# Performance work log

Measured on AMD Instinct MI355X. Metric: run time of the kernel, lower is better.

## Reference

```python
import jax, jax.numpy as jnp
import numpy as np

NA = 100000   # author nodes
NP = 100000   # paper nodes
E = 500000    # edges per relation
H = 128       # hidden size
FA = 256      # author input features
FP = 128      # paper input features
LA = 4        # author labels
LP = 7        # paper labels


def setup_inputs() -> dict:
    key = jax.random.key(0)
    ks = iter(jax.random.split(key, 48))
    def rn(shape, scale=0.05):
        return jax.random.normal(next(ks), shape, jnp.float32) * scale
    inp = {}
    inp['x_author'] = jax.random.normal(next(ks), (NA, FA), jnp.float32)
    inp['x_paper'] = jax.random.normal(next(ks), (NP, FP), jnp.float32)
    inp['edge_index_p2a'] = jax.random.randint(next(ks), (2, E), 0, 100000, jnp.int64)  # row0: paper src, row1: author dst
    inp['edge_index_a2p'] = jax.random.randint(next(ks), (2, E), 0, 100000, jnp.int64)  # row0: author src, row1: paper dst
    # layer 1 convs (per message type): lin_src, lin_dst, lin_update(2H->H)
    inp['w1_p2a_src'] = rn((FP, H)); inp['b1_p2a_src'] = rn((H,))
    inp['w1_p2a_dst'] = rn((FA, H)); inp['b1_p2a_dst'] = rn((H,))
    inp['w1_p2a_upd'] = rn((2 * H, H)); inp['b1_p2a_upd'] = rn((H,))
    inp['w1_a2p_src'] = rn((FA, H)); inp['b1_a2p_src'] = rn((H,))
    inp['w1_a2p_dst'] = rn((FP, H)); inp['b1_a2p_dst'] = rn((H,))
    inp['w1_a2p_upd'] = rn((2 * H, H)); inp['b1_a2p_upd'] = rn((H,))
    # layer 2 convs (all dims = H)
    inp['w2_p2a_src'] = rn((H, H)); inp['b2_p2a_src'] = rn((H,))
    inp['w2_p2a_dst'] = rn((H, H)); inp['b2_p2a_dst'] = rn((H,))
    inp['w2_p2a_upd'] = rn((2 * H, H)); inp['b2_p2a_upd'] = rn((H,))
    inp['w2_a2p_src'] = rn((H, H)); inp['b2_a2p_src'] = rn((H,))
    inp['w2_a2p_dst'] = rn((H, H)); inp['b2_a2p_dst'] = rn((H,))
    inp['w2_a2p_upd'] = rn((2 * H, H)); inp['b2_a2p_upd'] = rn((H,))
    # batchnorm affine params per node type per layer
    inp['g1_a'] = jnp.ones((H,), jnp.float32); inp['be1_a'] = jnp.zeros((H,), jnp.float32)
    inp['g1_p'] = jnp.ones((H,), jnp.float32); inp['be1_p'] = jnp.zeros((H,), jnp.float32)
    inp['g2_a'] = jnp.ones((H,), jnp.float32); inp['be2_a'] = jnp.zeros((H,), jnp.float32)
    inp['g2_p'] = jnp.ones((H,), jnp.float32); inp['be2_p'] = jnp.zeros((H,), jnp.float32)
    # post message-passing heads
    inp['w_post_a'] = rn((H, LA)); inp['b_post_a'] = rn((LA,))
    inp['w_post_p'] = rn((H, LP)); inp['b_post_p'] = rn((LP,))
    return inp


def _mean_agg(x_src, src, dst, n_dst):
    # gather source features along edges, mean-scatter to destination nodes
    msg = x_src[src]                                            # [E, F]
    s = jax.ops.segment_sum(msg, dst, num_segments=n_dst)       # [n_dst, F]
    cnt = jax.ops.segment_sum(jnp.ones((dst.shape[0],), msg.dtype), dst, num_segments=n_dst)
    return s / jnp.maximum(cnt, 1.0)[:, None]


def _conv(x_src, x_dst, src, dst, ws, bs, wd, bd, wu, bu):
    agg = _mean_agg(x_src, src, dst, x_dst.shape[0])
    h = jnp.concatenate([x_dst @ wd + bd, agg @ ws + bs], axis=-1)   # [n_dst, 2H]
    return h @ wu + bu


def _bn_lrelu(x, g, b):
    # BatchNorm1d(eps=1) in training mode (batch stats, biased var) then LeakyReLU(0.01)
    m = x.mean(axis=0)
    v = x.var(axis=0)
    y = g * (x - m) / jnp.sqrt(v + 1.0) + b
    return jnp.where(y >= 0, y, 0.01 * y)


def reference(x_author, x_paper, edge_index_p2a, edge_index_a2p,
              w1_p2a_src, b1_p2a_src, w1_p2a_dst, b1_p2a_dst, w1_p2a_upd, b1_p2a_upd,
              w1_a2p_src, b1_a2p_src, w1_a2p_dst, b1_a2p_dst, w1_a2p_upd, b1_a2p_upd,
              w2_p2a_src, b2_p2a_src, w2_p2a_dst, b2_p2a_dst, w2_p2a_upd, b2_p2a_upd,
              w2_a2p_src, b2_a2p_src, w2_a2p_dst, b2_a2p_dst, w2_a2p_upd, b2_a2p_upd,
              g1_a, be1_a, g1_p, be1_p, g2_a, be2_a, g2_p, be2_p,
              w_post_a, b_post_a, w_post_p, b_post_p):
    src_pa, dst_pa = edge_index_p2a[0], edge_index_p2a[1]
    src_ap, dst_ap = edge_index_a2p[0], edge_index_a2p[1]
    # layer 1: per-message-type conv -> per-node-type BN + LeakyReLU
    h_a = _conv(x_paper, x_author, src_pa, dst_pa, w1_p2a_src, b1_p2a_src, w1_p2a_dst, b1_p2a_dst, w1_p2a_upd, b1_p2a_upd)
    h_p = _conv(x_author, x_paper, src_ap, dst_ap, w1_a2p_src, b1_a2p_src, w1_a2p_dst, b1_a2p_dst, w1_a2p_upd, b1_a2p_upd)
    h_a = _bn_lrelu(h_a, g1_a, be1_a)
    h_p = _bn_lrelu(h_p, g1_p, be1_p)
    # layer 2
    h_a2 = _conv(h_p, h_a, src_pa, dst_pa, w2_p2a_src, b2_p2a_src, w2_p2a_dst, b2_p2a_dst, w2_p2a_upd, b2_p2a_upd)
    h_p2 = _conv(h_a, h_p, src_ap, dst_ap, w2_a2p_src, b2_a2p_src, w2_a2p_dst, b2_a2p_dst, w2_a2p_upd, b2_a2p_upd)
    h_a2 = _bn_lrelu(h_a2, g2_a, be2_a)
    h_p2 = _bn_lrelu(h_p2, g2_p, be2_p)
    # post message-passing heads per node type
    out_a = h_a2 @ w_post_a + b_post_a   # [NA, LA]
    out_p = h_p2 @ w_post_p + b_post_p   # [NP, LP]
    return (out_a, out_p)
```

## Files before the change

kernel.cpp:

```cpp
#include <hip/hip_runtime.h>

#define NN 100000
#define NE 500000
#define HD 128
#define NBLK 391

typedef float f32x4v __attribute__((ext_vector_type(4)));
typedef short s16x8  __attribute__((ext_vector_type(8)));

static __device__ __forceinline__ unsigned f2bf_bits(float f){
  unsigned u = __float_as_uint(f);
  return (u + 0x7FFF + ((u >> 16) & 1)) >> 16;
}

static __device__ __forceinline__ void split8(const float* a, s16x8& hi, s16x8& lo){
  #pragma unroll
  for (int j = 0; j < 8; ++j){
    float f = a[j];
    unsigned hb = f2bf_bits(f);
    float hf = __uint_as_float(hb << 16);
    float lf = f - hf;
    hi[j] = (short)hb;
    lo[j] = (short)f2bf_bits(lf);
  }
}

static __device__ __forceinline__ float4 bn_lrelu4(float4 v, float4 sc, float4 sh){
  v.x = v.x*sc.x + sh.x; v.x = v.x >= 0.f ? v.x : 0.01f*v.x;
  v.y = v.y*sc.y + sh.y; v.y = v.y >= 0.f ? v.y : 0.01f*v.y;
  v.z = v.z*sc.z + sh.z; v.z = v.z >= 0.f ? v.z : 0.01f*v.z;
  v.w = v.w*sc.w + sh.w; v.w = v.w >= 0.f ? v.w : 0.01f*v.w;
  return v;
}

__global__ void k_count(const int* __restrict__ ei_pa, const int* __restrict__ ei_ap,
                        int* __restrict__ deg2){
  int idx = blockIdx.x * 256 + threadIdx.x;
  if (idx < NE)        atomicAdd(&deg2[      ei_pa[NE + idx]], 1);
  else if (idx < 2*NE) atomicAdd(&deg2[NN + ei_ap[NE + (idx - NE)]], 1);
}

__global__ void k_bsum(const int* __restrict__ deg2, int* __restrict__ bsum){
  int rel = blockIdx.x / NBLK, b = blockIdx.x % NBLK;
  int i = b*256 + threadIdx.x;
  int v = (i < NN) ? deg2[rel*NN + i] : 0;
  __shared__ int s[256];
  s[threadIdx.x] = v; __syncthreads();
  for (int o = 128; o > 0; o >>= 1){
    if (threadIdx.x < o) s[threadIdx.x] += s[threadIdx.x + o];
    __syncthreads();
  }
  if (threadIdx.x == 0) bsum[rel*512 + b] = s[0];
}

__global__ void k_bscan(const int* __restrict__ bsum, int* __restrict__ bsoff){
  int rel = blockIdx.x, t = threadIdx.x;
  int v = (t < NBLK) ? bsum[rel*512 + t] : 0;
  __shared__ int s[512];
  s[t] = v; __syncthreads();
  for (int o = 1; o < 512; o <<= 1){
    int x = (t >= o) ? s[t - o] : 0;
    __syncthreads();
    s[t] += x;
    __syncthreads();
  }
  bsoff[rel*512 + t] = s[t] - v;
}

__global__ void k_scanC(const int* __restrict__ deg2, const int* __restrict__ bsoff,
                        int* __restrict__ off2, int* __restrict__ cur2){
  int rel = blockIdx.x / NBLK, b = blockIdx.x % NBLK;
  int i = b*256 + threadIdx.x, t = threadIdx.x;
  int v = (i < NN) ? deg2[rel*NN + i] : 0;
  __shared__ int s[256];
  s[t] = v; __syncthreads();
  for (int o = 1; o < 256; o <<= 1){
    int x = (t >= o) ? s[t - o] : 0;
    __syncthreads();
    s[t] += x;
    __syncthreads();
  }
  if (i < NN){
    int o = bsoff[rel*512 + b] + s[t] - v;
    off2[rel*NN + i] = o;
    cur2[rel*NN + i] = o;
  }
}

__global__ void k_fill(const int* __restrict__ ei_pa, const int* __restrict__ ei_ap,
                       int* __restrict__ cur2,
                       int* __restrict__ col_pa, int* __restrict__ col_ap){
  int idx = blockIdx.x * 256 + threadIdx.x;
  if (idx < NE){
    int s = ei_pa[idx], d = ei_pa[NE + idx];
    int pos = atomicAdd(&cur2[d], 1);
    col_pa[pos] = s;
  } else if (idx < 2*NE){
    int e = idx - NE;
    int s = ei_ap[e], d = ei_ap[NE + e];
    int pos = atomicAdd(&cur2[NN + d], 1);
    col_ap[pos] = s;
  }
}

struct FoldDesc { const float* A; const float* B; short* T; int off; };
struct FoldArgs { FoldDesc d[8]; int rs[9]; };

__global__ void k_fold(FoldArgs fa){
  int row = blockIdx.x;
  int seg = 0;
  #pragma unroll
  for (int s = 0; s < 8; ++s) if (row >= fa.rs[s+1]) seg = s + 1;
  int m = row - fa.rs[seg];
  const float* A = fa.d[seg].A + (size_t)m * 128;
  const float* B = fa.d[seg].B;
  int n = threadIdx.x;
  float acc = 0.f;
  for (int k = 0; k < 128; ++k) acc += A[k] * B[k*128 + n];
  unsigned hb = f2bf_bits(acc);
  float hf = __uint_as_float(hb << 16);
  unsigned lb = f2bf_bits(acc - hf);
  int gkc = fa.d[seg].off + (m >> 5), quad = (m >> 3) & 3, j = m & 7;
  int lane = quad*16 + (n & 15), nt = n >> 4;
  size_t fb = (size_t)((gkc*8 + nt)*2)*512 + lane*8 + j;
  fa.d[seg].T[fb]       = (short)hb;
  fa.d[seg].T[fb + 512] = (short)lb;
}

struct BiasArgs { const float* bd[4]; const float* bs[4]; const float* wu[4];
                  const float* bu[4]; float* outb[4]; };
__global__ void k_biasfold(BiasArgs ba){
  int s = blockIdx.x, j = threadIdx.x;
  const float* wu = ba.wu[s];
  float acc = ba.bu[s][j];
  for (int k = 0; k < 128; ++k)
    acc += ba.bd[s][k] * wu[k*128 + j] + ba.bs[s][k] * wu[(128 + k)*128 + j];
  ba.outb[s][j] = acc;
}

__global__ __launch_bounds__(256)
void k_gemm2(const float* __restrict__ A1, int lda1, int KC1,
             const float* __restrict__ bn1,
             const float* __restrict__ A2, int lda2, int KC2,
             const short* __restrict__ Bf,
             const float* __restrict__ bias, const float* __restrict__ extra,
             float* __restrict__ C, float* __restrict__ stats, int M)
{
  __shared__ __align__(16) char smem[32768];
  short* Bs = (short*)smem;

  const int tid  = threadIdx.x;
  const int wave = tid >> 6, lane = tid & 63;
  const int li   = lane & 15, quad = lane >> 4;
  const int rowT = blockIdx.x * 128 + wave * 32;
  const int KCtot = KC1 + KC2;

  f32x4v acc[2][8];
  #pragma unroll
  for (int mt = 0; mt < 2; ++mt)
    #pragma unroll
    for (int nt = 0; nt < 8; ++nt)
      acc[mt][nt] = (f32x4v){0.f, 0.f, 0.f, 0.f};

  float4 c0[2], c1[2], n0[2], n1[2];
  auto loadA = [&](int gkc, float4* p0, float4* p1){
    const float* Ab; int ld, kk; bool bn;
    if (gkc < KC1){ Ab = A1; ld = lda1; kk = gkc; bn = (bn1 != nullptr); }
    else          { Ab = A2; ld = lda2; kk = gkc - KC1; bn = false; }
    float4 sc0, sc1, sh0, sh1;
    if (bn){
      const float* bsc = bn1 + kk*32 + quad*8;
      sc0 = *(const float4*)bsc;        sc1 = *(const float4*)(bsc + 4);
      sh0 = *(const float4*)(bsc+128);  sh1 = *(const float4*)(bsc + 132);
    }
    #pragma unroll
    for (int mt = 0; mt < 2; ++mt){
      int row = rowT + mt*16 + li;
      if (row < M){
        const float* ap = Ab + (size_t)row*ld + kk*32 + quad*8;
        float4 v0 = *(const float4*)ap;
        float4 v1 = *(const float4*)(ap + 4);
        if (bn){ v0 = bn_lrelu4(v0, sc0, sh0); v1 = bn_lrelu4(v1, sc1, sh1); }
        p0[mt] = v0; p1[mt] = v1;
      } else {
        p0[mt] = make_float4(0.f,0.f,0.f,0.f);
        p1[mt] = make_float4(0.f,0.f,0.f,0.f);
      }
    }
  };
  loadA(0, c0, c1);

  for (int g = 0; g < KCtot; g += 2){
    if (g > 0) __syncthreads();
    const short* src = Bf + (size_t)g*8192;
    #pragma unroll
    for (int c2 = 0; c2 < 8; ++c2){
      int id = c2*256 + tid;
      *(s16x8*)(Bs + id*8) = *(const s16x8*)(src + id*8);
    }
    __syncthreads();
    #pragma unroll
    for (int kc = 0; kc < 2; ++kc){
      int gkc = g + kc;
      if (gkc + 1 < KCtot) loadA(gkc + 1, n0, n1);
      s16x8 ah[2], al[2];
      #pragma unroll
      for (int mt = 0; mt < 2; ++mt){
        float av[8] = {c0[mt].x, c0[mt].y, c0[mt].z, c0[mt].w,
                       c1[mt].x, c1[mt].y, c1[mt].z, c1[mt].w};
        split8(av, ah[mt], al[mt]);
      }
      #pragma unroll
      for (int nt = 0; nt < 8; ++nt){
        const short* bp = Bs + ((kc*8 + nt) << 10) + lane*8;
        s16x8 bh = *(const s16x8*)bp;
        s16x8 bl = *(const s16x8*)(bp + 512);
        #pragma unroll
        for (int mt = 0; mt < 2; ++mt){
          acc[mt][nt] = __builtin_amdgcn_mfma_f32_16x16x32_bf16(ah[mt], bh, acc[mt][nt], 0, 0, 0);
          acc[mt][nt] = __builtin_amdgcn_mfma_f32_16x16x32_bf16(al[mt], bh, acc[mt][nt], 0, 0, 0);
          acc[mt][nt] = __builtin_amdgcn_mfma_f32_16x16x32_bf16(ah[mt], bl, acc[mt][nt], 0, 0, 0);
        }
      }
      #pragma unroll
      for (int mt = 0; mt < 2; ++mt){ c0[mt] = n0[mt]; c1[mt] = n1[mt]; }
    }
  }

  __syncthreads();
  float* Cw = (float*)smem + wave*2048;
  int col4 = lane & 31;
  float4 bias4 = make_float4(0.f,0.f,0.f,0.f);
  if (bias) bias4 = ((const float4*)bias)[col4];
  float4 s1 = make_float4(0.f,0.f,0.f,0.f), s2 = s1;
  #pragma unroll
  for (int mt = 0; mt < 2; ++mt){
    #pragma unroll
    for (int r = 0; r < 4; ++r){
      int lr = quad*4 + r;
      #pragma unroll
      for (int nt = 0; nt < 8; ++nt){
        int c = nt*16 + li;
        int chunk = ((c >> 2) + 2*quad) & 31;
        Cw[lr*128 + chunk*4 + (c & 3)] = acc[mt][nt][r];
      }
    }
    #pragma unroll
    for (int i = 0; i < 8; ++i){
      int lr = i*2 + (lane >> 5);
      int grow = rowT + mt*16 + lr;
      if (grow >= M) continue;
      int chunk = (col4 + 2*(lr >> 2)) & 31;
      float4 v = *(const float4*)(Cw + lr*128 + chunk*4);
      v.x += bias4.x; v.y += bias4.y; v.z += bias4.z; v.w += bias4.w;
      if (extra){
        float4 e = ((const float4*)(extra + (size_t)grow*128))[col4];
        v.x += e.x; v.y += e.y; v.z += e.z; v.w += e.w;
      }
      ((float4*)(C + (size_t)grow*128))[col4] = v;
      s1.x += v.x; s1.y += v.y; s1.z += v.z; s1.w += v.w;
      s2.x += v.x*v.x; s2.y += v.y*v.y; s2.z += v.z*v.z; s2.w += v.w*v.w;
    }
  }
  if (stats){
    __syncthreads();
    float* Ss = (float*)smem;
    ((float4*)Ss)[tid*2]     = s1;
    ((float4*)Ss)[tid*2 + 1] = s2;
    __syncthreads();
    int c = tid & 127, kind = tid >> 7;
    int cc4 = c >> 2, comp = c & 3;
    float s = 0.f;
    #pragma unroll
    for (int wv = 0; wv < 4; ++wv)
      #pragma unroll
      for (int hf = 0; hf < 2; ++hf)
        s += Ss[(wv*64 + hf*32 + cc4)*8 + kind*4 + comp];
    atomicAdd(&stats[kind*128 + c], s);
  }
}

__global__ __launch_bounds__(256)
void k_agg(const float* __restrict__ t, const int* __restrict__ off,
           const int* __restrict__ deg, const int* __restrict__ col,
           float* __restrict__ o, const float* __restrict__ bn){
  int slot = threadIdx.x >> 5, col4 = threadIdx.x & 31;
  int d = blockIdx.x*8 + slot;
  if (d >= NN) return;
  float4 sc4, sh4;
  bool hasbn = (bn != nullptr);
  if (hasbn){ sc4 = ((const float4*)bn)[col4]; sh4 = ((const float4*)(bn+128))[col4]; }
  int s0 = off[d], cnt = deg[d];
  float4 a0 = make_float4(0.f,0.f,0.f,0.f), a1 = a0;
  int i = 0;
  for (; i + 4 <= cnt; i += 4){
    int sa = col[s0+i], sb = col[s0+i+1], sct = col[s0+i+2], sd = col[s0+i+3];
    float4 v0 = ((const float4*)(t + (size_t)sa*128))[col4];
    float4 v1 = ((const float4*)(t + (size_t)sb*128))[col4];
    float4 v2 = ((const float4*)(t + (size_t)sct*128))[col4];
    float4 v3 = ((const float4*)(t + (size_t)sd*128))[col4];
    if (hasbn){
      v0 = bn_lrelu4(v0, sc4, sh4); v1 = bn_lrelu4(v1, sc4, sh4);
      v2 = bn_lrelu4(v2, sc4, sh4); v3 = bn_lrelu4(v3, sc4, sh4);
    }
    a0.x += v0.x + v2.x; a0.y += v0.y + v2.y; a0.z += v0.z + v2.z; a0.w += v0.w + v2.w;
    a1.x += v1.x + v3.x; a1.y += v1.y + v3.y; a1.z += v1.z + v3.z; a1.w += v1.w + v3.w;
  }
  for (; i < cnt; ++i){
    int sa = col[s0+i];
    float4 v0 = ((const float4*)(t + (size_t)sa*128))[col4];
    if (hasbn) v0 = bn_lrelu4(v0, sc4, sh4);
    a0.x += v0.x; a0.y += v0.y; a0.z += v0.z; a0.w += v0.w;
  }
  float inv = 1.0f / (float)(cnt > 0 ? cnt : 1);
  float4 r;
  r.x = (a0.x + a1.x)*inv; r.y = (a0.y + a1.y)*inv;
  r.z = (a0.z + a1.z)*inv; r.w = (a0.w + a1.w)*inv;
  ((float4*)(o + (size_t)d*128))[col4] = r;
}

__global__ void k_bnprep(const float* __restrict__ stats, const float* __restrict__ g,
                         const float* __restrict__ b, float* __restrict__ sc, int M){
  int c = threadIdx.x;
  float invN = 1.0f / (float)M;
  float m  = stats[c] * invN;
  float var = stats[128 + c] * invN - m*m;
  float scale = g[c] / sqrtf(var + 1.0f);
  sc[c] = scale;
  sc[128 + c] = b[c] - m*scale;
}

template<int LC>
__global__ void k_head(const float* __restrict__ h, const float* __restrict__ bn,
                       const float* __restrict__ w, const float* __restrict__ b,
                       float* __restrict__ o, int M){
  __shared__ float ws[128*LC];
  __shared__ float bs[LC];
  __shared__ float bsc[256];
  for (int i = threadIdx.x; i < 128*LC; i += 256) ws[i] = w[i];
  if (threadIdx.x < LC) bs[threadIdx.x] = b[threadIdx.x];
  if (threadIdx.x < 256) bsc[threadIdx.x] = bn[threadIdx.x];
  __syncthreads();
  int r = blockIdx.x*256 + threadIdx.x;
  if (r >= M) return;
  float acc[LC];
  #pragma unroll
  for (int c = 0; c < LC; ++c) acc[c] = bs[c];
  const float4* hr = (const float4*)(h + (size_t)r*128);
  for (int k4 = 0; k4 < 32; ++k4){
    float4 v = hr[k4];
    float4 sc = ((const float4*)bsc)[k4];
    float4 sh = ((const float4*)bsc)[32 + k4];
    v = bn_lrelu4(v, sc, sh);
    int k = k4*4;
    #pragma unroll
    for (int c = 0; c < LC; ++c)
      acc[c] += v.x*ws[k*LC+c] + v.y*ws[(k+1)*LC+c] + v.z*ws[(k+2)*LC+c] + v.w*ws[(k+3)*LC+c];
  }
  #pragma unroll
  for (int c = 0; c < LC; ++c) o[(size_t)r*LC + c] = acc[c];
}

extern "C" void kernel_launch(void* const* d_in, const int* in_sizes, int n_in,
                              void* d_out, int out_size, void* d_ws, size_t ws_size,
                              hipStream_t stream) {
  const float* x_author = (const float*)d_in[0];
  const float* x_paper  = (const float*)d_in[1];
  const int*   ei_pa    = (const int*)d_in[2];
  const int*   ei_ap    = (const int*)d_in[3];

  char* p = (char*)d_ws;
  auto alloc = [&](size_t bytes) -> void* {
    void* r = (void*)p; p += (bytes + 255) & ~(size_t)255; return r;
  };
  short* T_l1a  = (short*)alloc(12u*16384);
  short* T_l1ps = (short*)alloc( 8u*16384);
  short* T_l1pd = (short*)alloc( 4u*16384);
  short* T_l2a  = (short*)alloc( 8u*16384);
  short* T_l2p  = (short*)alloc( 8u*16384);
  float* w1a_b = (float*)alloc(128*4);      float* w1p_b = (float*)alloc(128*4);
  float* w2a_b = (float*)alloc(128*4);      float* w2p_b = (float*)alloc(128*4);
  float* stats4 = (float*)alloc(4*256*4);
  float* bnsc4  = (float*)alloc(4*256*4);
  int* deg2  = (int*)alloc(2*NN*4);
  int* off2  = (int*)alloc(2*NN*4);
  int* cur2  = (int*)alloc(2*NN*4);
  int* col_pa = (int*)alloc(NE*4);
  int* col_ap = (int*)alloc(NE*4);
  int* bsum  = (int*)alloc(1024*4);
  int* bsoff = (int*)alloc(1024*4);
  const size_t NB = (size_t)NN * 128;
  float* B1 = (float*)alloc(NB*4);
  float* B2 = (float*)alloc(NB*4);
  float* B3 = (float*)alloc(NB*4);
  float* B4 = (float*)alloc(NB*4);

  hipMemsetAsync(deg2, 0, 2*NN*4, stream);
  hipMemsetAsync(stats4, 0, 4*256*4, stream);
  k_count<<<(2*NE + 255)/256, 256, 0, stream>>>(ei_pa, ei_ap, deg2);
  k_bsum <<<2*NBLK, 256, 0, stream>>>(deg2, bsum);
  k_bscan<<<2, 512, 0, stream>>>(bsum, bsoff);
  k_scanC<<<2*NBLK, 256, 0, stream>>>(deg2, bsoff, off2, cur2);
  k_fill <<<(2*NE + 255)/256, 256, 0, stream>>>(ei_pa, ei_ap, cur2, col_pa, col_ap);

  FoldArgs fa;
  const float* wu1a = (const float*)d_in[8];
  const float* wu1p = (const float*)d_in[14];
  const float* wu2a = (const float*)d_in[20];
  const float* wu2p = (const float*)d_in[26];
  fa.d[0] = { (const float*)d_in[6],  wu1a,           T_l1a,  0 };
  fa.d[1] = { (const float*)d_in[4],  wu1a + 128*128, T_l1a,  8 };
  fa.d[2] = { (const float*)d_in[10], wu1p + 128*128, T_l1ps, 0 };
  fa.d[3] = { (const float*)d_in[12], wu1p,           T_l1pd, 0 };
  fa.d[4] = { (const float*)d_in[18], wu2a,           T_l2a,  0 };
  fa.d[5] = { (const float*)d_in[16], wu2a + 128*128, T_l2a,  4 };
  fa.d[6] = { (const float*)d_in[24], wu2p,           T_l2p,  0 };
  fa.d[7] = { (const float*)d_in[22], wu2p + 128*128, T_l2p,  4 };
  int rows[8] = {256,128,256,128,128,128,128,128};
  fa.rs[0] = 0;
  for (int i = 0; i < 8; ++i) fa.rs[i+1] = fa.rs[i] + rows[i];
  k_fold<<<fa.rs[8], 128, 0, stream>>>(fa);

  BiasArgs ba;
  ba.bd[0]=(const float*)d_in[7];  ba.bs[0]=(const float*)d_in[5];  ba.wu[0]=wu1a; ba.bu[0]=(const float*)d_in[9];  ba.outb[0]=w1a_b;
  ba.bd[1]=(const float*)d_in[13]; ba.bs[1]=(const float*)d_in[11]; ba.wu[1]=wu1p; ba.bu[1]=(const float*)d_in[15]; ba.outb[1]=w1p_b;
  ba.bd[2]=(const float*)d_in[19]; ba.bs[2]=(const float*)d_in[17]; ba.wu[2]=wu2a; ba.bu[2]=(const float*)d_in[21]; ba.outb[2]=w2a_b;
  ba.bd[3]=(const float*)d_in[25]; ba.bs[3]=(const float*)d_in[23]; ba.wu[3]=wu2p; ba.bu[3]=(const float*)d_in[27]; ba.outb[3]=w2p_b;
  k_biasfold<<<4, 128, 0, stream>>>(ba);

  const int GG = (NN + 127)/128;
  const int AGG_GRID = (NN + 7)/8;
  const int* off_pa = off2;        const int* deg_pa = deg2;
  const int* off_ap = off2 + NN;   const int* deg_ap = deg2 + NN;
  float* st_a1 = stats4;       float* st_p1 = stats4 + 256;
  float* st_a2 = stats4 + 512; float* st_p2 = stats4 + 768;
  float* sc_a1 = bnsc4;        float* sc_p1 = bnsc4 + 256;
  float* sc_a2 = bnsc4 + 512;  float* sc_p2 = bnsc4 + 768;

  k_agg<<<AGG_GRID, 256, 0, stream>>>(x_paper, off_pa, deg_pa, col_pa, B4, nullptr);
  k_gemm2<<<GG, 256, 0, stream>>>(x_author, 256, 8, nullptr, B4, 128, 4, T_l1a,
                                  w1a_b, nullptr, B1, st_a1, NN);
  k_bnprep<<<1, 128, 0, stream>>>(st_a1, (const float*)d_in[28], (const float*)d_in[29], sc_a1, NN);

  k_gemm2<<<GG, 256, 0, stream>>>(x_author, 256, 8, nullptr, nullptr, 0, 0, T_l1ps,
                                  nullptr, nullptr, B3, nullptr, NN);
  k_agg<<<AGG_GRID, 256, 0, stream>>>(B3, off_ap, deg_ap, col_ap, B4, nullptr);
  k_gemm2<<<GG, 256, 0, stream>>>(x_paper, 128, 4, nullptr, nullptr, 0, 0, T_l1pd,
                                  w1p_b, B4, B2, st_p1, NN);
  k_bnprep<<<1, 128, 0, stream>>>(st_p1, (const float*)d_in[30], (const float*)d_in[31], sc_p1, NN);

  k_agg<<<AGG_GRID, 256, 0, stream>>>(B2, off_pa, deg_pa, col_pa, B4, sc_p1);
  k_gemm2<<<GG, 256, 0, stream>>>(B1, 128, 4, sc_a1, B4, 128, 4, T_l2a,
                                  w2a_b, nullptr, B3, st_a2, NN);
  k_bnprep<<<1, 128, 0, stream>>>(st_a2, (const float*)d_in[32], (const float*)d_in[33], sc_a2, NN);
  k_head<4><<<(NN + 255)/256, 256, 0, stream>>>(B3, sc_a2, (const float*)d_in[36],
                                                (const float*)d_in[37], (float*)d_out, NN);

  k_agg<<<AGG_GRID, 256, 0, stream>>>(B1, off_ap, deg_ap, col_ap, B4, sc_a1);
  k_gemm2<<<GG, 256, 0, stream>>>(B2, 128, 4, sc_p1, B4, 128, 4, T_l2p,
                                  w2p_b, nullptr, B3, st_p2, NN);
  k_bnprep<<<1, 128, 0, stream>>>(st_p2, (const float*)d_in[34], (const float*)d_in[35], sc_p2, NN);
  k_head<7><<<(NN + 255)/256, 256, 0, stream>>>(B3, sc_p2, (const float*)d_in[38],
                                                (const float*)d_in[39], (float*)d_out + (size_t)NN*4, NN);
}
```

Before: 862.0 us.

## Store intermediates as pre-split bf16 hi/lo pairs and stage B via LDS DMA

Intermediate activation buffers now hold each row as bf16 hi and lo halves instead of fp32. The GEMM can then feed MFMA directly without re-splitting in the inner loop, and aggregation reconstructs fp32 from the halves. BatchNorm+LeakyReLU is moved into a separate in-place pass (k_bnapply) rather than being applied inside agg and GEMM loads. B tiles are loaded with global_load_lds and A prefetch is restructured into double-buffered two-chunk phases. Total bytes per buffer are unchanged. The change adds extra kernel passes, and the split/reconstruct steps carry a small precision risk.

```diff
diff --git a/kernel.cpp b/kernel.cpp
--- a/kernel.cpp
+++ b/kernel.cpp
@@ -12,16 +12,32 @@
   unsigned u = __float_as_uint(f);
   return (u + 0x7FFF + ((u >> 16) & 1)) >> 16;
 }
-
-static __device__ __forceinline__ void split8(const float* a, s16x8& hi, s16x8& lo){
-  #pragma unroll
-  for (int j = 0; j < 8; ++j){
-    float f = a[j];
+static __device__ __forceinline__ float bfu(unsigned short u){
+  return __uint_as_float(((unsigned)u) << 16);
+}
+static __device__ __forceinline__ float4 recon4(ushort4 h, ushort4 l){
+  return make_float4(bfu(h.x)+bfu(l.x), bfu(h.y)+bfu(l.y),
+                     bfu(h.z)+bfu(l.z), bfu(h.w)+bfu(l.w));
+}
+static __device__ __forceinline__ void split4(float4 v, ushort4& h, ushort4& l){
+  unsigned hb;
+  hb = f2bf_bits(v.x); h.x = (unsigned short)hb; l.x = (unsigned short)f2bf_bits(v.x - __uint_as_float(hb<<16));
+  hb = f2bf_bits(v.y); h.y = (unsigned short)hb; l.y = (unsigned short)f2bf_bits(v.y - __uint_as_float(hb<<16));
+  hb = f2bf_bits(v.z); h.z = (unsigned short)hb; l.z = (unsigned short)f2bf_bits(v.z - __uint_as_float(hb<<16));
+  hb = f2bf_bits(v.w); h.w = (unsigned short)hb; l.w = (unsigned short)f2bf_bits(v.w - __uint_as_float(hb<<16));
+}
+static __device__ __forceinline__ void split8v(f32x4v v0, f32x4v v1, s16x8& hi, s16x8& lo){
+  #pragma unroll
+  for (int j = 0; j < 4; ++j){
+    float f = v0[j];
     unsigned hb = f2bf_bits(f);
-    float hf = __uint_as_float(hb << 16);
-    float lf = f - hf;
-    hi[j] = (short)hb;
-    lo[j] = (short)f2bf_bits(lf);
+    hi[j] = (short)hb; lo[j] = (short)f2bf_bits(f - __uint_as_float(hb << 16));
+  }
+  #pragma unroll
+  for (int j = 0; j < 4; ++j){
+    float f = v1[j];
+    unsigned hb = f2bf_bits(f);
+    hi[4+j] = (short)hb; lo[4+j] = (short)f2bf_bits(f - __uint_as_float(hb << 16));
   }
 }
 
@@ -138,13 +154,13 @@
   ba.outb[s][j] = acc;
 }
 
+template<int SPLITA1>
 __global__ __launch_bounds__(256)
-void k_gemm2(const float* __restrict__ A1, int lda1, int KC1,
-             const float* __restrict__ bn1,
-             const float* __restrict__ A2, int lda2, int KC2,
+void k_gemm2(const void* __restrict__ A1v, int K1, int KC1,
+             const ushort* __restrict__ A2, int K2, int KC2,
              const short* __restrict__ Bf,
-             const float* __restrict__ bias, const float* __restrict__ extra,
-             float* __restrict__ C, float* __restrict__ stats, int M)
+             const float* __restrict__ bias, const ushort* __restrict__ extra,
+             ushort* __restrict__ C, float* __restrict__ stats, int M)
 {
   __shared__ __align__(16) char smem[32768];
   short* Bs = (short*)smem;
@@ -162,53 +178,71 @@
     for (int nt = 0; nt < 8; ++nt)
       acc[mt][nt] = (f32x4v){0.f, 0.f, 0.f, 0.f};
 
-  float4 c0[2], c1[2], n0[2], n1[2];
-  auto loadA = [&](int gkc, float4* p0, float4* p1){
-    const float* Ab; int ld, kk; bool bn;
-    if (gkc < KC1){ Ab = A1; ld = lda1; kk = gkc; bn = (bn1 != nullptr); }
-    else          { Ab = A2; ld = lda2; kk = gkc - KC1; bn = false; }
-    float4 sc0, sc1, sh0, sh1;
-    if (bn){
-      const float* bsc = bn1 + kk*32 + quad*8;
-      sc0 = *(const float4*)bsc;        sc1 = *(const float4*)(bsc + 4);
-      sh0 = *(const float4*)(bsc+128);  sh1 = *(const float4*)(bsc + 132);
-    }
-    #pragma unroll
-    for (int mt = 0; mt < 2; ++mt){
-      int row = rowT + mt*16 + li;
-      if (row < M){
-        const float* ap = Ab + (size_t)row*ld + kk*32 + quad*8;
-        float4 v0 = *(const float4*)ap;
-        float4 v1 = *(const float4*)(ap + 4);
-        if (bn){ v0 = bn_lrelu4(v0, sc0, sh0); v1 = bn_lrelu4(v1, sc1, sh1); }
-        p0[mt] = v0; p1[mt] = v1;
-      } else {
-        p0[mt] = make_float4(0.f,0.f,0.f,0.f);
-        p1[mt] = make_float4(0.f,0.f,0.f,0.f);
+  const char*   b1[2];
+  const ushort* b2[2];
+  #pragma unroll
+  for (int mt = 0; mt < 2; ++mt){
+    int row = rowT + mt*16 + li;
+    int r = (row < M) ? row : 0;
+    if (SPLITA1) b1[mt] = (const char*)((const ushort*)A1v + (size_t)r*(2*K1) + quad*8);
+    else         b1[mt] = (const char*)((const float*) A1v + (size_t)r*K1     + quad*8);
+    b2[mt] = A2 ? (A2 + (size_t)r*(2*K2) + quad*8) : (const ushort*)nullptr;
+  }
+
+  f32x4v aA[2][2][2], aB[2][2][2];
+
+  auto loadA = [&](int g, f32x4v (&dst)[2][2][2]){
+    #pragma unroll
+    for (int kc = 0; kc < 2; ++kc){
+      int gkc = g + kc;
+      #pragma unroll
+      for (int mt = 0; mt < 2; ++mt){
+        if (gkc < KC1){
+          if (SPLITA1){
+            const ushort* p = (const ushort*)b1[mt] + gkc*32;
+            dst[kc][mt][0] = *(const f32x4v*)p;
+            dst[kc][mt][1] = *(const f32x4v*)(p + K1);
+          } else {
+            const float* p = (const float*)b1[mt] + gkc*32;
+            dst[kc][mt][0] = *(const f32x4v*)p;
+            dst[kc][mt][1] = *(const f32x4v*)(p + 4);
+          }
+        } else {
+          const ushort* p = b2[mt] + (gkc - KC1)*32;
+          dst[kc][mt][0] = *(const f32x4v*)p;
+          dst[kc][mt][1] = *(const f32x4v*)(p + K2);
+        }
       }
     }
   };
-  loadA(0, c0, c1);
-
-  for (int g = 0; g < KCtot; g += 2){
-    if (g > 0) __syncthreads();
-    const short* src = Bf + (size_t)g*8192;
-    #pragma unroll
-    for (int c2 = 0; c2 < 8; ++c2){
-      int id = c2*256 + tid;
-      *(s16x8*)(Bs + id*8) = *(const s16x8*)(src + id*8);
+
+  auto stageB = [&](int g){
+    const char* s = (const char*)Bf + (size_t)g * 16384;
+    #pragma unroll
+    for (int c = 0; c < 8; ++c){
+      int blk = wave*8 + c;
+      __builtin_amdgcn_global_load_lds(
+          (const __attribute__((address_space(1))) unsigned int*)(s + blk*1024 + lane*16),
+          (__attribute__((address_space(3))) unsigned int*)(smem + blk*1024),
+          16, 0, 0);
     }
-    __syncthreads();
+  };
+
+  auto computeG = [&](int g, f32x4v (&a)[2][2][2]){
+    bool f32g = (!SPLITA1) && (g < KC1);
     #pragma unroll
     for (int kc = 0; kc < 2; ++kc){
-      int gkc = g + kc;
-      if (gkc + 1 < KCtot) loadA(gkc + 1, n0, n1);
       s16x8 ah[2], al[2];
-      #pragma unroll
-      for (int mt = 0; mt < 2; ++mt){
-        float av[8] = {c0[mt].x, c0[mt].y, c0[mt].z, c0[mt].w,
-                       c1[mt].x, c1[mt].y, c1[mt].z, c1[mt].w};
-        split8(av, ah[mt], al[mt]);
+      if (f32g){
+        #pragma unroll
+        for (int mt = 0; mt < 2; ++mt)
+          split8v(a[kc][mt][0], a[kc][mt][1], ah[mt], al[mt]);
+      } else {
+        #pragma unroll
+        for (int mt = 0; mt < 2; ++mt){
+          ah[mt] = __builtin_bit_cast(s16x8, a[kc][mt][0]);
+          al[mt] = __builtin_bit_cast(s16x8, a[kc][mt][1]);
+        }
       }
       #pragma unroll
       for (int nt = 0; nt < 8; ++nt){
@@ -222,9 +256,21 @@
           acc[mt][nt] = __builtin_amdgcn_mfma_f32_16x16x32_bf16(ah[mt], bl, acc[mt][nt], 0, 0, 0);
         }
       }
-      #pragma unroll
-      for (int mt = 0; mt < 2; ++mt){ c0[mt] = n0[mt]; c1[mt] = n1[mt]; }
     }
+  };
+
+  auto phase = [&](int G, f32x4v (&cur)[2][2][2], f32x4v (&nxt)[2][2][2]){
+    if (G) __syncthreads();
+    stageB(G);
+    __syncthreads();
+    if (G + 2 < KCtot) loadA(G + 2, nxt);
+    computeG(G, cur);
+  };
+
+  loadA(0, aA);
+  for (int g = 0; g < KCtot; g += 4){
+    phase(g,     aA, aB);
+    phase(g + 2, aB, aA);
   }
 
   __syncthreads();
@@ -254,10 +300,16 @@
       float4 v = *(const float4*)(Cw + lr*128 + chunk*4);
       v.x += bias4.x; v.y += bias4.y; v.z += bias4.z; v.w += bias4.w;
       if (extra){
-        float4 e = ((const float4*)(extra + (size_t)grow*128))[col4];
+        const ushort* er = extra + ((size_t)grow << 8) + col4*4;
+        ushort4 eh = *(const ushort4*)er;
+        ushort4 el = *(const ushort4*)(er + 128);
+        float4 e = recon4(eh, el);
         v.x += e.x; v.y += e.y; v.z += e.z; v.w += e.w;
       }
-      ((float4*)(C + (size_t)grow*128))[col4] = v;
+      ushort4 h4, l4; split4(v, h4, l4);
+      ushort* cr = C + ((size_t)grow << 8) + col4*4;
+      *(ushort4*)cr = h4;
+      *(ushort4*)(cr + 128) = l4;
       s1.x += v.x; s1.y += v.y; s1.z += v.z; s1.w += v.w;
       s2.x += v.x*v.x; s2.y += v.y*v.y; s2.z += v.z*v.z; s2.w += v.w*v.w;
     }
@@ -280,43 +332,50 @@
   }
 }
 
+template<int IS>
 __global__ __launch_bounds__(256)
-void k_agg(const float* __restrict__ t, const int* __restrict__ off,
+void k_agg(const void* __restrict__ tv, const int* __restrict__ off,
            const int* __restrict__ deg, const int* __restrict__ col,
-           float* __restrict__ o, const float* __restrict__ bn){
+           ushort* __restrict__ o){
+  const float*  tf = (const float*)tv;
+  const ushort* ts = (const ushort*)tv;
   int slot = threadIdx.x >> 5, col4 = threadIdx.x & 31;
   int d = blockIdx.x*8 + slot;
   if (d >= NN) return;
-  float4 sc4, sh4;
-  bool hasbn = (bn != nullptr);
-  if (hasbn){ sc4 = ((const float4*)bn)[col4]; sh4 = ((const float4*)(bn+128))[col4]; }
+  auto loadrow = [&](int row) -> float4 {
+    if (IS){
+      const ushort* p = ts + ((size_t)row << 8) + col4*4;
+      ushort4 h = *(const ushort4*)p;
+      ushort4 l = *(const ushort4*)(p + 128);
+      return recon4(h, l);
+    } else {
+      return ((const float4*)(tf + ((size_t)row << 7)))[col4];
+    }
+  };
   int s0 = off[d], cnt = deg[d];
   float4 a0 = make_float4(0.f,0.f,0.f,0.f), a1 = a0;
   int i = 0;
   for (; i + 4 <= cnt; i += 4){
     int sa = col[s0+i], sb = col[s0+i+1], sct = col[s0+i+2], sd = col[s0+i+3];
-    float4 v0 = ((const float4*)(t + (size_t)sa*128))[col4];
-    float4 v1 = ((const float4*)(t + (size_t)sb*128))[col4];
-    float4 v2 = ((const float4*)(t + (size_t)sct*128))[col4];
-    float4 v3 = ((const float4*)(t + (size_t)sd*128))[col4];
-    if (hasbn){
-      v0 = bn_lrelu4(v0, sc4, sh4); v1 = bn_lrelu4(v1, sc4, sh4);
-      v2 = bn_lrelu4(v2, sc4, sh4); v3 = bn_lrelu4(v3, sc4, sh4);
-    }
+    float4 v0 = loadrow(sa);
+    float4 v1 = loadrow(sb);
+    float4 v2 = loadrow(sct);
+    float4 v3 = loadrow(sd);
     a0.x += v0.x + v2.x; a0.y += v0.y + v2.y; a0.z += v0.z + v2.z; a0.w += v0.w + v2.w;
     a1.x += v1.x + v3.x; a1.y += v1.y + v3.y; a1.z += v1.z + v3.z; a1.w += v1.w + v3.w;
   }
   for (; i < cnt; ++i){
-    int sa = col[s0+i];
-    float4 v0 = ((const float4*)(t + (size_t)sa*128))[col4];
-    if (hasbn) v0 = bn_lrelu4(v0, sc4, sh4);
+    float4 v0 = loadrow(col[s0+i]);
     a0.x += v0.x; a0.y += v0.y; a0.z += v0.z; a0.w += v0.w;
   }
   float inv = 1.0f / (float)(cnt > 0 ? cnt : 1);
   float4 r;
   r.x = (a0.x + a1.x)*inv; r.y = (a0.y + a1.y)*inv;
   r.z = (a0.z + a1.z)*inv; r.w = (a0.w + a1.w)*inv;
-  ((float4*)(o + (size_t)d*128))[col4] = r;
+  ushort4 h4, l4; split4(r, h4, l4);
+  ushort* po = o + ((size_t)d << 8) + col4*4;
+  *(ushort4*)po = h4;
+  *(ushort4*)(po + 128) = l4;
 }
 
 __global__ void k_bnprep(const float* __restrict__ stats, const float* __restrict__ g,
@@ -330,8 +389,24 @@
   sc[128 + c] = b[c] - m*scale;
 }
 
+__global__ __launch_bounds__(256)
+void k_bnapply(ushort* __restrict__ t, const float* __restrict__ bn){
+  int i = blockIdx.x*256 + threadIdx.x;
+  int row = i >> 5, c4 = i & 31;
+  float4 sc = ((const float4*)bn)[c4];
+  float4 sh = ((const float4*)(bn + 128))[c4];
+  ushort* p = t + ((size_t)row << 8) + c4*4;
+  ushort4 h = *(const ushort4*)p;
+  ushort4 l = *(const ushort4*)(p + 128);
+  float4 v = recon4(h, l);
+  v = bn_lrelu4(v, sc, sh);
+  split4(v, h, l);
+  *(ushort4*)p = h;
+  *(ushort4*)(p + 128) = l;
+}
+
 template<int LC>
-__global__ void k_head(const float* __restrict__ h, const float* __restrict__ bn,
+__global__ void k_head(const ushort* __restrict__ h, const float* __restrict__ bn,
                        const float* __restrict__ w, const float* __restrict__ b,
                        float* __restrict__ o, int M){
   __shared__ float ws[128*LC];
@@ -346,9 +421,11 @@
   float acc[LC];
   #pragma unroll
   for (int c = 0; c < LC; ++c) acc[c] = bs[c];
-  const float4* hr = (const float4*)(h + (size_t)r*128);
+  const ushort* hr = h + ((size_t)r << 8);
   for (int k4 = 0; k4 < 32; ++k4){
-    float4 v = hr[k4];
+    ushort4 uh = ((const ushort4*)hr)[k4];
+    ushort4 ul = ((const ushort4*)(hr + 128))[k4];
+    float4 v = recon4(uh, ul);
     float4 sc = ((const float4*)bsc)[k4];
     float4 sh = ((const float4*)bsc)[32 + k4];
     v = bn_lrelu4(v, sc, sh);
@@ -390,10 +467,10 @@
   int* bsum  = (int*)alloc(1024*4);
   int* bsoff = (int*)alloc(1024*4);
   const size_t NB = (size_t)NN * 128;
-  float* B1 = (float*)alloc(NB*4);
-  float* B2 = (float*)alloc(NB*4);
-  float* B3 = (float*)alloc(NB*4);
-  float* B4 = (float*)alloc(NB*4);
+  ushort* B1 = (ushort*)alloc(NB*4);
+  ushort* B2 = (ushort*)alloc(NB*4);
+  ushort* B3 = (ushort*)alloc(NB*4);
+  ushort* B4 = (ushort*)alloc(NB*4);
 
   hipMemsetAsync(deg2, 0, 2*NN*4, stream);
   hipMemsetAsync(stats4, 0, 4*256*4, stream);
@@ -430,6 +507,7 @@
 
   const int GG = (NN + 127)/128;
   const int AGG_GRID = (NN + 7)/8;
+  const int BN_GRID  = (NN*32)/256;
   const int* off_pa = off2;        const int* deg_pa = deg2;
   const int* off_ap = off2 + NN;   const int* deg_ap = deg2 + NN;
   float* st_a1 = stats4;       float* st_p1 = stats4 + 256;
@@ -437,28 +515,31 @@
   float* sc_a1 = bnsc4;        float* sc_p1 = bnsc4 + 256;
   float* sc_a2 = bnsc4 + 512;  float* sc_p2 = bnsc4 + 768;
 
-  k_agg<<<AGG_GRID, 256, 0, stream>>>(x_paper, off_pa, deg_pa, col_pa, B4, nullptr);
-  k_gemm2<<<GG, 256, 0, stream>>>(x_author, 256, 8, nullptr, B4, 128, 4, T_l1a,
-                                  w1a_b, nullptr, B1, st_a1, NN);
+  k_agg<0><<<AGG_GRID, 256, 0, stream>>>(x_paper, off_pa, deg_pa, col_pa, B4);
+  k_gemm2<0><<<GG, 256, 0, stream>>>(x_author, 256, 8, B4, 128, 4, T_l1a,
+                                     w1a_b, nullptr, B1, st_a1, NN);
   k_bnprep<<<1, 128, 0, stream>>>(st_a1, (const float*)d_in[28], (const float*)d_in[29], sc_a1, NN);
 
-  k_gemm2<<<GG, 256, 0, stream>>>(x_author, 256, 8, nullptr, nullptr, 0, 0, T_l1ps,
-                                  nullptr, nullptr, B3, nullptr, NN);
-  k_agg<<<AGG_GRID, 256, 0, stream>>>(B3, off_ap, deg_ap, col_ap, B4, nullptr);
-  k_gemm2<<<GG, 256, 0, stream>>>(x_paper, 128, 4, nullptr, nullptr, 0, 0, T_l1pd,
-                                  w1p_b, B4, B2, st_p1, NN);
+  k_gemm2<0><<<GG, 256, 0, stream>>>(x_author, 256, 8, nullptr, 0, 0, T_l1ps,
+                                     nullptr, nullptr, B3, nullptr, NN);
+  k_agg<1><<<AGG_GRID, 256, 0, stream>>>(B3, off_ap, deg_ap, col_ap, B4);
+  k_gemm2<0><<<GG, 256, 0, stream>>>(x_paper, 128, 4, nullptr, 0, 0, T_l1pd,
+                                     w1p_b, B4, B2, st_p1, NN);
   k_bnprep<<<1, 128, 0, stream>>>(st_p1, (const float*)d_in[30], (const float*)d_in[31], sc_p1, NN);
 
-  k_agg<<<AGG_GRID, 256, 0, stream>>>(B2, off_pa, deg_pa, col_pa, B4, sc_p1);
-  k_gemm2<<<GG, 256, 0, stream>>>(B1, 128, 4, sc_a1, B4, 128, 4, T_l2a,
-                                  w2a_b, nullptr, B3, st_a2, NN);
+  k_bnapply<<<BN_GRID, 256, 0, stream>>>(B1, sc_a1);
+  k_bnapply<<<BN_GRID, 256, 0, stream>>>(B2, sc_p1);
+
+  k_agg<1><<<AGG_GRID, 256, 0, stream>>>(B2, off_pa, deg_pa, col_pa, B4);
+  k_gemm2<1><<<GG, 256, 0, stream>>>(B1, 128, 4, B4, 128, 4, T_l2a,
+                                     w2a_b, nullptr, B3, st_a2, NN);
   k_bnprep<<<1, 128, 0, stream>>>(st_a2, (const float*)d_in[32], (const float*)d_in[33], sc_a2, NN);
   k_head<4><<<(NN + 255)/256, 256, 0, stream>>>(B3, sc_a2, (const float*)d_in[36],
                                                 (const float*)d_in[37], (float*)d_out, NN);
 
-  k_agg<<<AGG_GRID, 256, 0, stream>>>(B1, off_ap, deg_ap, col_ap, B4, sc_a1);
-  k_gemm2<<<GG, 256, 0, stream>>>(B2, 128, 4, sc_p1, B4, 128, 4, T_l2p,
-                                  w2p_b, nullptr, B3, st_p2, NN);
+  k_agg<1><<<AGG_GRID, 256, 0, stream>>>(B1, off_ap, deg_ap, col_ap, B4);
+  k_gemm2<1><<<GG, 256, 0, stream>>>(B2, 128, 4, B4, 128, 4, T_l2p,
+                                     w2p_b, nullptr, B3, st_p2, NN);
   k_bnprep<<<1, 128, 0, stream>>>(st_p2, (const float*)d_in[34], (const float*)d_in[35], sc_p2, NN);
   k_head<7><<<(NN + 255)/256, 256, 0, stream>>>(B3, sc_p2, (const float*)d_in[38],
                                                 (const float*)d_in[39], (float*)d_out + (size_t)NN*4, NN);
```

Measured after the change: 922.6 us. 7.0% more time.
